# Optimization experiments

Measured on AMD Instinct MI355X. Metric: run time of the kernel, lower is better.

Reference implementation:

```python
import jax, jax.numpy as jnp
import numpy as np

EPS = 1e-8  # torch F.cosine_similarity eps


def _normalize(x):
    # x: [N, D]; clamp norm at eps like torch cosine_similarity
    n = jnp.linalg.norm(x, axis=-1, keepdims=True)
    return x / jnp.maximum(n, EPS)


def setup_inputs() -> dict:
    key = jax.random.key(0)
    k1, k2 = jax.random.split(key)
    N, D = 8192, 256
    return {
        "model_output": jax.random.normal(k1, (N, D), dtype=jnp.float32),
        "targets": jax.random.normal(k2, (N, D), dtype=jnp.float32),
        "weight": 1.0,
    }


def reference(model_output, targets, weight):
    # Pairwise cosine similarity via normalize + matmul (same math as
    # broadcasted cosine_similarity, without the O(N^2*D) intermediate).
    o = _normalize(model_output)          # [N, D]
    t = _normalize(targets)               # [N, D]
    sim_o = o @ o.T                       # [N, N]
    sim_t = t @ t.T                       # [N, N]
    n = sim_o.shape[0]
    mask = jnp.eye(n, dtype=bool)
    sim_o = jnp.where(mask, 0.0, sim_o)
    sim_t = jnp.where(mask, 0.0, sim_t)
    loss = jnp.mean((sim_o - sim_t) ** 2)
    return weight * loss
```

## Files before the change

### kernel.cpp

```cpp
#include <hip/hip_runtime.h>
#include <hip/hip_bf16.h>
#include <math.h>


#define N_ROWS 8192
#define DDIM   256
#define NC     32
#define KC     (N_ROWS / NC)
#define KS     64
#define NITER  (KC / KS)
#define PART_STRIDE 196608

#define OBT_UOFF  32
#define MAT_USZ   (DDIM * N_ROWS)
#define PART_UOFF (OBT_UOFF + 2 * MAT_USZ)

typedef __bf16 bf16x8 __attribute__((ext_vector_type(8)));
typedef short  short8 __attribute__((ext_vector_type(8)));
typedef float  f32x16 __attribute__((ext_vector_type(16)));
typedef unsigned int u32;

__device__ inline unsigned short f2bu(float x) {
    __hip_bfloat16 h = __float2bfloat16(x);
    return __builtin_bit_cast(unsigned short, h);
}
__device__ inline float u2f(unsigned short u) {
    unsigned int v = ((unsigned int)u) << 16;
    return __builtin_bit_cast(float, v);
}
__device__ inline void gload_lds16(const void* g, void* l) {
    __builtin_amdgcn_global_load_lds(
        (const __attribute__((address_space(1))) u32*)g,
        (__attribute__((address_space(3))) u32*)l, 16, 0, 0);
}

__global__ __launch_bounds__(256) void transpose_kernel(const float* __restrict__ O,
                                                        const float* __restrict__ T,
                                                        float* __restrict__ ws) {
    if (blockIdx.x == 0 && threadIdx.x == 0) ws[0] = 0.0f;
    int b = blockIdx.x;
    const float* src = (b & 1) ? T : O;
    unsigned short* dst = (unsigned short*)ws + OBT_UOFF + (size_t)(b & 1) * MAT_USZ;
    int kb = (b >> 1) * 32;
    __shared__ unsigned short lt[32][260];
    int w = threadIdx.x >> 6, l = threadIdx.x & 63;
    #pragma unroll
    for (int j = 0; j < 8; ++j) {
        int r = j * 4 + w;
        float4 v = *reinterpret_cast<const float4*>(src + (size_t)(kb + r) * DDIM + l * 4);
        float ss = v.x * v.x + v.y * v.y + v.z * v.z + v.w * v.w;
        #pragma unroll
        for (int off = 32; off > 0; off >>= 1) ss += __shfl_xor(ss, off);
        float inv = 1.0f / fmaxf(sqrtf(ss), 1e-8f);
        ushort4 u;
        u.x = f2bu(v.x * inv); u.y = f2bu(v.y * inv);
        u.z = f2bu(v.z * inv); u.w = f2bu(v.w * inv);
        *reinterpret_cast<ushort4*>(&lt[r][l * 4]) = u;
    }
    __syncthreads();
    int f = threadIdx.x;
    #pragma unroll
    for (int s = 0; s < 8; ++s) {
        ushort4 u;
        u.x = lt[s * 4 + 0][f]; u.y = lt[s * 4 + 1][f];
        u.z = lt[s * 4 + 2][f]; u.w = lt[s * 4 + 3][f];
        *reinterpret_cast<ushort4*>(&dst[(size_t)f * N_ROWS + kb + s * 4]) = u;
    }
}

__global__ __launch_bounds__(256) void gram_kernel(float* __restrict__ ws) {
    const unsigned short* obt = (const unsigned short*)ws + OBT_UOFF;
    unsigned short* part = (unsigned short*)ws + PART_UOFF;

    int bid = blockIdx.x;
    int ti = bid & 15, c = bid >> 4;
    int tm = ti >> 2, tn = ti & 3;
    int tid = threadIdx.x, lane = tid & 63, wid = tid >> 6;
    int wm = wid >> 1, wn = wid & 1;
    int k0 = c * KC;

    __shared__ __align__(16) unsigned short lds[2][4][KS * 64];

    f32x16 acc_oo, acc_tt, acc_ot;
    #pragma unroll
    for (int e = 0; e < 16; ++e) { acc_oo[e] = 0.f; acc_tt[e] = 0.f; acc_ot[e] = 0.f; }

    int sl = wid;
    int mat = sl >> 1;
    int ft = (sl & 1) ? tn : tm;
    const unsigned short* slab_src =
        obt + (size_t)mat * MAT_USZ + (size_t)(ft * 64) * N_ROWS;
    int frow = lane >> 3;
    int swz8 = ((lane & 7) ^ (frow & 7)) * 8;

    auto stage = [&](int buf, int it) {
        int kb = k0 + it * KS;
        const unsigned short* base = slab_src + kb + (size_t)frow * N_ROWS + swz8;
        unsigned short* ld = &lds[buf][sl][0];
        #pragma unroll
        for (int i = 0; i < 8; ++i)
            gload_lds16(base + (size_t)(i * 8) * N_ROWS, ld + i * 512);
    };

    int fm = wm * 32 + (lane & 31);
    int fn = wn * 32 + (lane & 31);
    int jhalf = lane >> 5;
    auto frag = [&](int buf, int s, int fl, int kk) -> bf16x8 {
        int j0 = kk * 2 + jhalf;
        const unsigned short* p = &lds[buf][s][fl * 64 + ((j0 ^ (fl & 7)) * 8)];
        return __builtin_bit_cast(bf16x8, *reinterpret_cast<const short8*>(p));
    };

    stage(0, 0);
    __syncthreads();
    int cur = 0;
    for (int it = 0; it < NITER; ++it) {
        if (it + 1 < NITER) stage(cur ^ 1, it + 1);
        #pragma unroll
        for (int kk = 0; kk < 4; ++kk) {
            bf16x8 ao = frag(cur, 0, fm, kk);
            bf16x8 bo = frag(cur, 1, fn, kk);
            bf16x8 at = frag(cur, 2, fm, kk);
            bf16x8 bt = frag(cur, 3, fn, kk);
            acc_oo = __builtin_amdgcn_mfma_f32_32x32x16_bf16(ao, bo, acc_oo, 0, 0, 0);
            acc_tt = __builtin_amdgcn_mfma_f32_32x32x16_bf16(at, bt, acc_tt, 0, 0, 0);
            acc_ot = __builtin_amdgcn_mfma_f32_32x32x16_bf16(ao, bt, acc_ot, 0, 0, 0);
        }
        __syncthreads();
        cur ^= 1;
    }

    unsigned int tb = (unsigned int)(c * 16 + ti) * 3;
    #pragma unroll
    for (int reg = 0; reg < 16; ++reg) {
        int row = (reg & 3) + 8 * (reg >> 2) + ((lane >> 5) << 2);
        int col = lane & 31;
        int idx = (wm * 32 + row) * 64 + (wn * 32 + col);
        part[(size_t)(tb + 0) * 4096 + idx] = f2bu(acc_oo[reg]);
        part[(size_t)(tb + 1) * 4096 + idx] = f2bu(acc_tt[reg]);
        part[(size_t)(tb + 2) * 4096 + idx] = f2bu(acc_ot[reg]);
    }
}

__global__ void reduce_kernel(float* __restrict__ ws) {
    const unsigned short* part = (const unsigned short*)ws + PART_UOFF;
    int gid = blockIdx.x * blockDim.x + threadIdx.x;
    int base = gid * 4;
    float s0 = 0.f, s1 = 0.f, s2 = 0.f, s3 = 0.f;
    for (int cc = 0; cc < NC; ++cc) {
        ushort4 u = *reinterpret_cast<const ushort4*>(&part[(size_t)cc * PART_STRIDE + base]);
        s0 += u2f(u.x); s1 += u2f(u.y); s2 += u2f(u.z); s3 += u2f(u.w);
    }
    int g = (base >> 12) % 3;
    float s = s0 * s0 + s1 * s1 + s2 * s2 + s3 * s3;
    if (g == 2) s = -2.0f * s;
    #pragma unroll
    for (int off = 32; off > 0; off >>= 1) s += __shfl_down(s, off);
    __shared__ float wsum[4];
    int lane = threadIdx.x & 63, w = threadIdx.x >> 6;
    if (lane == 0) wsum[w] = s;
    __syncthreads();
    if (threadIdx.x == 0)
        atomicAdd(&ws[0], wsum[0] + wsum[1] + wsum[2] + wsum[3]);
}

__global__ void finalize_kernel(const float* __restrict__ ws,
                                const float* __restrict__ weight,
                                float* __restrict__ out) {
    out[0] = ws[0] * weight[0] / ((float)N_ROWS * (float)N_ROWS);
}

extern "C" void kernel_launch(void* const* d_in, const int* in_sizes, int n_in,
                              void* d_out, int out_size, void* d_ws, size_t ws_size,
                              hipStream_t stream) {
    const float* O = (const float*)d_in[0];
    const float* T = (const float*)d_in[1];
    const float* W = (const float*)d_in[2];
    float* out = (float*)d_out;
    float* ws = (float*)d_ws;

    transpose_kernel<<<512, 256, 0, stream>>>(O, T, ws);
    gram_kernel<<<16 * NC, 256, 0, stream>>>(ws);
    reduce_kernel<<<192, 256, 0, stream>>>(ws);
    finalize_kernel<<<1, 1, 0, stream>>>(ws, W, out);
}
```

Baseline: 31.39 us.

## Fuse reduce and finalize into gram kernel with atomic grid barrier

Merges the reduce and finalize kernels into the gram kernel. Every block bumps a completion counter, and the first 192 blocks spin until all 512 have arrived, then reduce the partials; the last reducer writes the output. The transpose is rewritten to cover 64 rows per block with a swizzled LDS layout and 16-byte stores, and the gram K-step shrinks from 64 to 32 with matching swizzle changes. This removes two kernel launches at the cost of a spin-wait that assumes all 512 blocks can be resident at once, plus smaller per-iteration tiles and more loop iterations.

```diff
diff --git a/kernel.cpp b/kernel.cpp
--- a/kernel.cpp
+++ b/kernel.cpp
@@ -7,9 +7,11 @@
 #define DDIM   256
 #define NC     32
 #define KC     (N_ROWS / NC)
-#define KS     64
+#define KS     32
 #define NITER  (KC / KS)
 #define PART_STRIDE 196608
+#define NGRAM  512
+#define NRED   192
 
 #define OBT_UOFF  32
 #define MAT_USZ   (DDIM * N_ROWS)
@@ -17,6 +19,7 @@
 
 typedef __bf16 bf16x8 __attribute__((ext_vector_type(8)));
 typedef short  short8 __attribute__((ext_vector_type(8)));
+typedef unsigned short ushort8 __attribute__((ext_vector_type(8)));
 typedef float  f32x16 __attribute__((ext_vector_type(16)));
 typedef unsigned int u32;
 
@@ -37,17 +40,25 @@
 __global__ __launch_bounds__(256) void transpose_kernel(const float* __restrict__ O,
                                                         const float* __restrict__ T,
                                                         float* __restrict__ ws) {
-    if (blockIdx.x == 0 && threadIdx.x == 0) ws[0] = 0.0f;
+    int tid = threadIdx.x;
+    if (blockIdx.x == 0 && tid == 0) {
+        ws[0] = 0.0f;
+        ((u32*)(ws + 4))[0] = 0u;
+        ((u32*)(ws + 4))[1] = 0u;
+    }
     int b = blockIdx.x;
     const float* src = (b & 1) ? T : O;
-    unsigned short* dst = (unsigned short*)ws + OBT_UOFF + (size_t)(b & 1) * MAT_USZ;
-    int kb = (b >> 1) * 32;
-    __shared__ unsigned short lt[32][260];
-    int w = threadIdx.x >> 6, l = threadIdx.x & 63;
-    #pragma unroll
-    for (int j = 0; j < 8; ++j) {
+    unsigned short* dst =
+        (unsigned short*)ws + OBT_UOFF + (size_t)(b & 1) * MAT_USZ;
+    int kb = (b >> 1) * 64;
+
+    __shared__ unsigned short lt[64 * 256];
+    int w = tid >> 6, l = tid & 63;
+    #pragma unroll
+    for (int j = 0; j < 16; ++j) {
         int r = j * 4 + w;
-        float4 v = *reinterpret_cast<const float4*>(src + (size_t)(kb + r) * DDIM + l * 4);
+        float4 v = *reinterpret_cast<const float4*>(
+            src + (size_t)(kb + r) * DDIM + l * 4);
         float ss = v.x * v.x + v.y * v.y + v.z * v.z + v.w * v.w;
         #pragma unroll
         for (int off = 32; off > 0; off >>= 1) ss += __shfl_xor(ss, off);
@@ -55,22 +66,30 @@
         ushort4 u;
         u.x = f2bu(v.x * inv); u.y = f2bu(v.y * inv);
         u.z = f2bu(v.z * inv); u.w = f2bu(v.w * inv);
-        *reinterpret_cast<ushort4*>(&lt[r][l * 4]) = u;
-    }
-    __syncthreads();
-    int f = threadIdx.x;
+        int idx = r * 256 + ((((l >> 1) ^ (r & 31)) << 3) | ((l & 1) << 2));
+        *reinterpret_cast<ushort4*>(&lt[idx]) = u;
+    }
+    __syncthreads();
     #pragma unroll
     for (int s = 0; s < 8; ++s) {
-        ushort4 u;
-        u.x = lt[s * 4 + 0][f]; u.y = lt[s * 4 + 1][f];
-        u.z = lt[s * 4 + 2][f]; u.w = lt[s * 4 + 3][f];
-        *reinterpret_cast<ushort4*>(&dst[(size_t)f * N_ROWS + kb + s * 4]) = u;
-    }
-}
-
-__global__ __launch_bounds__(256) void gram_kernel(float* __restrict__ ws) {
+        int f = (tid >> 3) + 32 * s;
+        int kc = tid & 7;
+        ushort8 u;
+        #pragma unroll
+        for (int j = 0; j < 8; ++j) {
+            int k = kc * 8 + j;
+            u[j] = lt[k * 256 + ((((f >> 3) ^ (k & 31)) << 3) | (f & 7))];
+        }
+        *reinterpret_cast<ushort8*>(&dst[(size_t)f * N_ROWS + kb + kc * 8]) = u;
+    }
+}
+
+__global__ __launch_bounds__(256) void gram_kernel(const float* __restrict__ W,
+                                                   float* __restrict__ out,
+                                                   float* __restrict__ ws) {
     const unsigned short* obt = (const unsigned short*)ws + OBT_UOFF;
     unsigned short* part = (unsigned short*)ws + PART_UOFF;
+    u32* ctr = (u32*)(ws + 4);
 
     int bid = blockIdx.x;
     int ti = bid & 15, c = bid >> 4;
@@ -79,7 +98,8 @@
     int wm = wid >> 1, wn = wid & 1;
     int k0 = c * KC;
 
-    __shared__ __align__(16) unsigned short lds[2][4][KS * 64];
+    __shared__ __align__(16) unsigned short slabs[2][4][64 * KS];
+    __shared__ float wsum[4];
 
     f32x16 acc_oo, acc_tt, acc_ot;
     #pragma unroll
@@ -88,18 +108,18 @@
     int sl = wid;
     int mat = sl >> 1;
     int ft = (sl & 1) ? tn : tm;
+    int frow = lane >> 2;
+    int koct = lane & 3;
     const unsigned short* slab_src =
-        obt + (size_t)mat * MAT_USZ + (size_t)(ft * 64) * N_ROWS;
-    int frow = lane >> 3;
-    int swz8 = ((lane & 7) ^ (frow & 7)) * 8;
+        obt + (size_t)mat * MAT_USZ + (size_t)(ft * 64 + frow) * N_ROWS
+        + ((koct ^ (frow & 3)) * 8);
 
     auto stage = [&](int buf, int it) {
         int kb = k0 + it * KS;
-        const unsigned short* base = slab_src + kb + (size_t)frow * N_ROWS + swz8;
-        unsigned short* ld = &lds[buf][sl][0];
-        #pragma unroll
-        for (int i = 0; i < 8; ++i)
-            gload_lds16(base + (size_t)(i * 8) * N_ROWS, ld + i * 512);
+        unsigned short* ld = &slabs[buf][sl][0];
+        #pragma unroll
+        for (int i = 0; i < 4; ++i)
+            gload_lds16(slab_src + kb + (size_t)(i * 16) * N_ROWS, ld + i * 512);
     };
 
     int fm = wm * 32 + (lane & 31);
@@ -107,7 +127,7 @@
     int jhalf = lane >> 5;
     auto frag = [&](int buf, int s, int fl, int kk) -> bf16x8 {
         int j0 = kk * 2 + jhalf;
-        const unsigned short* p = &lds[buf][s][fl * 64 + ((j0 ^ (fl & 7)) * 8)];
+        const unsigned short* p = &slabs[buf][s][fl * KS + ((j0 ^ (fl & 3)) * 8)];
         return __builtin_bit_cast(bf16x8, *reinterpret_cast<const short8*>(p));
     };
 
@@ -117,7 +137,7 @@
     for (int it = 0; it < NITER; ++it) {
         if (it + 1 < NITER) stage(cur ^ 1, it + 1);
         #pragma unroll
-        for (int kk = 0; kk < 4; ++kk) {
+        for (int kk = 0; kk < 2; ++kk) {
             bf16x8 ao = frag(cur, 0, fm, kk);
             bf16x8 bo = frag(cur, 1, fn, kk);
             bf16x8 at = frag(cur, 2, fm, kk);
@@ -140,34 +160,50 @@
         part[(size_t)(tb + 1) * 4096 + idx] = f2bu(acc_tt[reg]);
         part[(size_t)(tb + 2) * 4096 + idx] = f2bu(acc_ot[reg]);
     }
-}
-
-__global__ void reduce_kernel(float* __restrict__ ws) {
-    const unsigned short* part = (const unsigned short*)ws + PART_UOFF;
-    int gid = blockIdx.x * blockDim.x + threadIdx.x;
-    int base = gid * 4;
-    float s0 = 0.f, s1 = 0.f, s2 = 0.f, s3 = 0.f;
-    for (int cc = 0; cc < NC; ++cc) {
-        ushort4 u = *reinterpret_cast<const ushort4*>(&part[(size_t)cc * PART_STRIDE + base]);
-        s0 += u2f(u.x); s1 += u2f(u.y); s2 += u2f(u.z); s3 += u2f(u.w);
-    }
-    int g = (base >> 12) % 3;
-    float s = s0 * s0 + s1 * s1 + s2 * s2 + s3 * s3;
-    if (g == 2) s = -2.0f * s;
-    #pragma unroll
-    for (int off = 32; off > 0; off >>= 1) s += __shfl_down(s, off);
-    __shared__ float wsum[4];
-    int lane = threadIdx.x & 63, w = threadIdx.x >> 6;
-    if (lane == 0) wsum[w] = s;
-    __syncthreads();
-    if (threadIdx.x == 0)
-        atomicAdd(&ws[0], wsum[0] + wsum[1] + wsum[2] + wsum[3]);
-}
-
-__global__ void finalize_kernel(const float* __restrict__ ws,
-                                const float* __restrict__ weight,
-                                float* __restrict__ out) {
-    out[0] = ws[0] * weight[0] / ((float)N_ROWS * (float)N_ROWS);
+
+    __syncthreads();
+    if (tid == 0) {
+        __threadfence();
+        atomicAdd(&ctr[0], 1u);
+    }
+    if (bid >= NRED) return;
+
+    if (tid == 0) {
+        while (__hip_atomic_load(&ctr[0], __ATOMIC_ACQUIRE,
+                                 __HIP_MEMORY_SCOPE_AGENT) < NGRAM)
+            __builtin_amdgcn_s_sleep(2);
+    }
+    __syncthreads();
+    __threadfence();
+
+    {
+        int gid = bid * 256 + tid;
+        int base = gid * 4;
+        float s0 = 0.f, s1 = 0.f, s2 = 0.f, s3 = 0.f;
+        for (int cc = 0; cc < NC; ++cc) {
+            ushort4 u = *reinterpret_cast<const ushort4*>(
+                &part[(size_t)cc * PART_STRIDE + base]);
+            s0 += u2f(u.x); s1 += u2f(u.y); s2 += u2f(u.z); s3 += u2f(u.w);
+        }
+        int g = (base >> 12) % 3;
+        float s = s0 * s0 + s1 * s1 + s2 * s2 + s3 * s3;
+        if (g == 2) s = -2.0f * s;
+        #pragma unroll
+        for (int off = 32; off > 0; off >>= 1) s += __shfl_down(s, off);
+        int l = tid & 63, w = tid >> 6;
+        if (l == 0) wsum[w] = s;
+        __syncthreads();
+        if (tid == 0) {
+            atomicAdd(&ws[0], wsum[0] + wsum[1] + wsum[2] + wsum[3]);
+            __threadfence();
+            unsigned int r = atomicAdd(&ctr[1], 1u);
+            if (r == NRED - 1) {
+                float v = __hip_atomic_load(&ws[0], __ATOMIC_ACQUIRE,
+                                            __HIP_MEMORY_SCOPE_AGENT);
+                out[0] = v * W[0] / ((float)N_ROWS * (float)N_ROWS);
+            }
+        }
+    }
 }
 
 extern "C" void kernel_launch(void* const* d_in, const int* in_sizes, int n_in,
@@ -179,8 +215,6 @@
     float* out = (float*)d_out;
     float* ws = (float*)d_ws;
 
-    transpose_kernel<<<512, 256, 0, stream>>>(O, T, ws);
-    gram_kernel<<<16 * NC, 256, 0, stream>>>(ws);
-    reduce_kernel<<<192, 256, 0, stream>>>(ws);
-    finalize_kernel<<<1, 1, 0, stream>>>(ws, W, out);
-}
+    transpose_kernel<<<256, 256, 0, stream>>>(O, T, ws);
+    gram_kernel<<<NGRAM, 256, 0, stream>>>(W, out, ws);
+}
```

Measured after the change: 94.10 us. 3x slower.
